# Kernel tuning notes

Hardware: AMD Instinct MI355X
Metric: run time of the kernel (lower is better)

Reference implementation:

```python
import jax, jax.numpy as jnp
import numpy as np

B, L, D, H = 8, 2048, 128, 128
MASK_VALUE = -1e30


def setup_inputs() -> dict:
    key = jax.random.key(0)
    ks = jax.random.split(key, 5)
    return {
        "query": jax.random.normal(ks[0], (B, L, D), dtype=jnp.float32),
        "key": jax.random.normal(ks[1], (B, L, D), dtype=jnp.float32),
        "value": jax.random.normal(ks[2], (B, L, D), dtype=jnp.float32),
        "mask": jnp.ones((B, L), dtype=jnp.float32),
        "Wq": jax.random.normal(ks[3], (D, H), dtype=jnp.float32) * (1.0 / np.sqrt(D)),
        "Wk": jax.random.normal(ks[4], (D, H), dtype=jnp.float32) * (1.0 / np.sqrt(D)),
    }


def reference(query, key, value, mask, Wq, Wk):
    # q: [B,Lq,H], k: [B,Lk,H]
    q = jnp.einsum("bqd,dh->bqh", query, Wq)
    k = jnp.einsum("bkd,dh->bkh", key, Wk)
    # unscaled scores [B,Lq,Lk]
    A = jnp.einsum("bqh,bkh->bqk", q, k)
    m = mask[:, None, :]  # [B,1,Lk]
    A = m * A + (1.0 - m) * MASK_VALUE
    # inference path: no dropout (learning_phase False)
    A = jax.nn.softmax(A, axis=-1)
    return jnp.einsum("bqk,bkd->bqd", A, value)
```

## Files before the change

kernel.cpp:

```cpp
#include <hip/hip_runtime.h>

#define NB 8
#define NL 2048
#define ND 128
#define NH 128
#define MASKVAL (-1e30f)
#define SHIFTC 40.0f

typedef __attribute__((ext_vector_type(8))) short short8;
typedef __attribute__((ext_vector_type(4))) float f32x4;

__device__ __forceinline__ unsigned short bf16_rn(float f) {
  unsigned u = __float_as_uint(f);
  u += 0x7fffu + ((u >> 16) & 1u);
  return (unsigned short)(u >> 16);
}
__device__ __forceinline__ float bf16_tof(unsigned short h) {
  return __uint_as_float(((unsigned)h) << 16);
}
__device__ __forceinline__ void gload16(const void* g, void* l) {
  __builtin_amdgcn_global_load_lds(
      (const __attribute__((address_space(1))) unsigned*)g,
      (__attribute__((address_space(3))) unsigned*)l, 16, 0, 0);
}


__global__ __launch_bounds__(256) void wprep_kernel(
    const float* __restrict__ Wq, const float* __restrict__ Wk,
    short* __restrict__ wthq, short* __restrict__ wtlq,
    short* __restrict__ wthk, short* __restrict__ wtlk)
{
  int m = blockIdx.x >> 4;
  int bb = blockIdx.x & 15;
  const float* W = m ? Wk : Wq;
  short* wth = m ? wthk : wthq;
  short* wtl = m ? wtlk : wtlq;
  int idx = bb * 256 + threadIdx.x;
  int d = idx >> 5, hc = idx & 31;
  float4 wv = *(const float4*)(W + d * NH + hc * 4);
  float vv[4] = {wv.x, wv.y, wv.z, wv.w};
#pragma unroll
  for (int j = 0; j < 4; ++j) {
    int h = hc * 4 + j;
    unsigned short hb = bf16_rn(vv[j]);
    unsigned short lb = bf16_rn(vv[j] - bf16_tof(hb));
    wth[h * ND + d] = (short)hb;
    wtl[h * ND + d] = (short)lb;
  }
}

__global__ __launch_bounds__(256) void vtprep_kernel(
    const float* __restrict__ value, short* __restrict__ kvs)
{
  __shared__ short Tl[64][66];
  __shared__ short VB[2][2048];
  int b = blockIdx.x >> 6;
  int k0 = ((blockIdx.x >> 1) & 31) * 64;
  int d0 = (blockIdx.x & 1) * 64;
  int t = threadIdx.x;
  int dm = t & 7, kp = t >> 3;
  float v0[8], v1[8];
  {
    const float* vp0 = value + (size_t)(b * NL + k0 + kp * 2) * ND + d0 + dm * 8;
    const float* vp1 = vp0 + ND;
    float4 a0 = *(const float4*)vp0;       float4 c0 = *(const float4*)(vp0 + 4);
    float4 a1 = *(const float4*)vp1;       float4 c1 = *(const float4*)(vp1 + 4);
    v0[0]=a0.x; v0[1]=a0.y; v0[2]=a0.z; v0[3]=a0.w; v0[4]=c0.x; v0[5]=c0.y; v0[6]=c0.z; v0[7]=c0.w;
    v1[0]=a1.x; v1[1]=a1.y; v1[2]=a1.z; v1[3]=a1.w; v1[4]=c1.x; v1[5]=c1.y; v1[6]=c1.z; v1[7]=c1.w;
  }
#pragma unroll
  for (int j = 0; j < 8; ++j) {
    unsigned pk = (unsigned)bf16_rn(v0[j]) | ((unsigned)bf16_rn(v1[j]) << 16);
    *(unsigned*)&Tl[dm * 8 + j][kp * 2] = pk;
  }
  __syncthreads();
  int dr = t >> 2, kc4 = t & 3;
  int d = d0 + dr;
  const unsigned* base = (const unsigned*)&Tl[dr][0];
  unsigned w[8];
#pragma unroll
  for (int i = 0; i < 8; ++i) w[i] = base[kc4 * 8 + i];
  int jt = kc4 >> 1;
  int kcg = (kc4 & 1) * 2;
  int g0 = ((d * 4 + kcg) ^ (d & 7)) - d0 * 4;
  int g1 = ((d * 4 + kcg + 1) ^ (d & 7)) - d0 * 4;
  *(uint4*)&VB[jt][g0 * 8] = make_uint4(w[0], w[1], w[2], w[3]);
  *(uint4*)&VB[jt][g1 * 8] = make_uint4(w[4], w[5], w[6], w[7]);
  __syncthreads();
  int kt = k0 >> 5;
#pragma unroll
  for (int c = 0; c < 2; ++c) {
    int idx = c * 256 + t;
    int j = idx >> 8, off = (idx & 255) * 8;
    *(uint4*)(kvs + (size_t)(b * 64 + kt + j) * 12288 + 8192 + d0 * 32 + off) =
        *(const uint4*)&VB[j][off];
  }
}

__global__ __launch_bounds__(256) void proj_kernel(
    const float* __restrict__ query, const float* __restrict__ key,
    const short* __restrict__ wthq, const short* __restrict__ wtlq,
    const short* __restrict__ wthk, const short* __restrict__ wtlk,
    unsigned* __restrict__ qhl, short* __restrict__ kvs)
{
  __shared__ short KB2[16384];
  const float* X = blockIdx.y ? key : query;
  const short* wth = blockIdx.y ? wthk : wthq;
  const short* wtl = blockIdx.y ? wtlk : wtlq;

  int tid = threadIdx.x;
  int wave = tid >> 6, lane = tid & 63;
  int lr = lane & 15, dg = lane >> 4;
  int arow = blockIdx.x * 64 + wave * 16 + lr;

  short8 ah[4], al[4];
  const float* xr = X + (size_t)arow * ND;
#pragma unroll
  for (int ks = 0; ks < 4; ++ks) {
    float4 a0 = *(const float4*)(xr + ks * 32 + dg * 8);
    float4 a1 = *(const float4*)(xr + ks * 32 + dg * 8 + 4);
    float vv[8] = {a0.x, a0.y, a0.z, a0.w, a1.x, a1.y, a1.z, a1.w};
    short8 h, l;
#pragma unroll
    for (int j = 0; j < 8; ++j) {
      unsigned short hb = bf16_rn(vv[j]);
      h[j] = (short)hb;
      l[j] = (short)bf16_rn(vv[j] - bf16_tof(hb));
    }
    ah[ks] = h; al[ks] = l;
  }

#pragma unroll
  for (int cf = 0; cf < 8; ++cf) {
    f32x4 acc = {0.f, 0.f, 0.f, 0.f};
    int col = cf * 16 + lr;
    const short* whp = wth + (size_t)col * ND;
    const short* wlp = wtl + (size_t)col * ND;
#pragma unroll
    for (int ks = 0; ks < 4; ++ks) {
      short8 wh = *(const short8*)(whp + ks * 32 + dg * 8);
      short8 wl = *(const short8*)(wlp + ks * 32 + dg * 8);
      acc = __builtin_amdgcn_mfma_f32_16x16x32_bf16(ah[ks], wh, acc, 0, 0, 0);
      acc = __builtin_amdgcn_mfma_f32_16x16x32_bf16(al[ks], wh, acc, 0, 0, 0);
      acc = __builtin_amdgcn_mfma_f32_16x16x32_bf16(ah[ks], wl, acc, 0, 0, 0);
    }
#pragma unroll
    for (int r = 0; r < 4; ++r) {
      int orow = blockIdx.x * 64 + wave * 16 + dg * 4 + r;
      float v = acc[r];
      unsigned short hb = bf16_rn(v);
      unsigned short lb = bf16_rn(v - bf16_tof(hb));
      if (blockIdx.y == 0) {
        qhl[(size_t)orow * NH + col] = ((unsigned)lb << 16) | (unsigned)hb;
      } else {
        int jj = (orow >> 5) & 1;
        int krow = orow & 31;
        int gr = krow * 128 + (((col >> 3) ^ (krow & 7)) * 8) + (col & 7);
        KB2[jj * 8192 + gr] = (short)hb;
        KB2[jj * 8192 + 4096 + gr] = (short)lb;
      }
    }
  }
  if (blockIdx.y == 1) {
    __syncthreads();
    int r0 = blockIdx.x * 64;
    int bb2 = r0 >> 11;
    int kt0 = (r0 & (NL - 1)) >> 5;
#pragma unroll
    for (int c = 0; c < 8; ++c) {
      int idx = c * 256 + tid;
      int j = idx >> 10, off = (idx & 1023) * 8;
      *(uint4*)(kvs + (size_t)(bb2 * 64 + kt0 + j) * 12288 + off) =
          *(const uint4*)&KB2[j * 8192 + off];
    }
  }
}

__global__ __launch_bounds__(256, 2) void attn_kernel(
    const unsigned* __restrict__ qhl, const short* __restrict__ kvs,
    const float* __restrict__ mask,
    unsigned short* __restrict__ pacc, float* __restrict__ pl)
{
  __shared__ short KV[2][12288];
  __shared__ float Msk[1024];
  __shared__ short Plds[4][16][32];

  int tid = threadIdx.x;
  int w = tid >> 6, lane = tid & 63;
  int lr = lane & 15, dg = lane >> 4;
  int b = blockIdx.x & 7;
  int qt = (blockIdx.x >> 3) & 31;
  int half = blockIdx.x >> 8;
  int q0 = qt * 64;

  short8 qh[4], ql[4];
  {
    const unsigned* qp = qhl + (size_t)(b * NL + q0 + w * 16 + lr) * NH;
#pragma unroll
    for (int ks = 0; ks < 4; ++ks) {
      uint4 u0 = *(const uint4*)(qp + ks * 32 + dg * 8);
      uint4 u1 = *(const uint4*)(qp + ks * 32 + dg * 8 + 4);
      unsigned uv[8] = {u0.x, u0.y, u0.z, u0.w, u1.x, u1.y, u1.z, u1.w};
      short8 h, l;
#pragma unroll
      for (int j = 0; j < 8; ++j) {
        h[j] = (short)(uv[j] & 0xffffu);
        l[j] = (short)(uv[j] >> 16);
      }
      qh[ks] = h; ql[ks] = l;
    }
  }

  gload16(mask + b * NL + half * 1024 + w * 256 + lane * 4, Msk + w * 256);

  f32x4 accv[8];
#pragma unroll
  for (int f = 0; f < 8; ++f) accv[f] = (f32x4){0.f, 0.f, 0.f, 0.f};
  float lrow[4] = {0.f, 0.f, 0.f, 0.f};

  const short* gbase = kvs + (size_t)(b * 64 + half * 32) * 12288 + w * 3072 + lane * 8;

#pragma unroll
  for (int i = 0; i < 6; ++i)
    gload16(gbase + i * 512, &KV[0][w * 3072 + i * 512]);

  for (int t = 0; t < 32; ++t) {
    __builtin_amdgcn_s_barrier();
    if (t + 1 < 32) {
      const short* gt = gbase + (size_t)(t + 1) * 12288;
      short* lt = &KV[(t + 1) & 1][w * 3072];
#pragma unroll
      for (int i = 0; i < 6; ++i)
        gload16(gt + i * 512, lt + i * 512);
      asm volatile("s_waitcnt vmcnt(6)" ::: "memory");
    } else {
      asm volatile("s_waitcnt vmcnt(0)" ::: "memory");
    }
    __builtin_amdgcn_s_barrier();
    __builtin_amdgcn_sched_barrier(0);

    const short* Kb = &KV[t & 1][0];
    f32x4 sc0 = {0.f, 0.f, 0.f, 0.f}, sc1 = {0.f, 0.f, 0.f, 0.f};
#pragma unroll
    for (int ks = 0; ks < 4; ++ks) {
      int chp = (((ks * 4 + dg) ^ (lr & 7)) * 8);
      short8 b0h = *(const short8*)(Kb + lr * 128 + chp);
      short8 b0l = *(const short8*)(Kb + 4096 + lr * 128 + chp);
      short8 b1h = *(const short8*)(Kb + (16 + lr) * 128 + chp);
      short8 b1l = *(const short8*)(Kb + 4096 + (16 + lr) * 128 + chp);
      sc0 = __builtin_amdgcn_mfma_f32_16x16x32_bf16(qh[ks], b0h, sc0, 0, 0, 0);
      sc1 = __builtin_amdgcn_mfma_f32_16x16x32_bf16(qh[ks], b1h, sc1, 0, 0, 0);
      sc0 = __builtin_amdgcn_mfma_f32_16x16x32_bf16(ql[ks], b0h, sc0, 0, 0, 0);
      sc1 = __builtin_amdgcn_mfma_f32_16x16x32_bf16(ql[ks], b1h, sc1, 0, 0, 0);
      sc0 = __builtin_amdgcn_mfma_f32_16x16x32_bf16(qh[ks], b0l, sc0, 0, 0, 0);
      sc1 = __builtin_amdgcn_mfma_f32_16x16x32_bf16(qh[ks], b1l, sc1, 0, 0, 0);
    }
    float mk0 = Msk[t * 32 + lr];
    float mk1 = Msk[t * 32 + 16 + lr];
#pragma unroll
    for (int r = 0; r < 4; ++r) {
      float s0 = mk0 * sc0[r] + (1.f - mk0) * MASKVAL - SHIFTC;
      float s1 = mk1 * sc1[r] + (1.f - mk1) * MASKVAL - SHIFTC;
      float p0 = __expf(s0);
      float p1 = __expf(s1);
      lrow[r] += p0 + p1;
      Plds[w][dg * 4 + r][lr] = (short)bf16_rn(p0);
      Plds[w][dg * 4 + r][16 + lr] = (short)bf16_rn(p1);
    }
    short8 pa = *(const short8*)&Plds[w][lr][dg * 8];
#pragma unroll
    for (int f = 0; f < 8; ++f) {
      int row = f * 16 + lr;
      int cp = (((row * 4 + dg) ^ (row & 7)) * 8);
      short8 bv = *(const short8*)(Kb + 8192 + cp);
      accv[f] = __builtin_amdgcn_mfma_f32_16x16x32_bf16(pa, bv, accv[f], 0, 0, 0);
    }
  }

#pragma unroll
  for (int r = 0; r < 4; ++r) {
    float lt = lrow[r];
    lt += __shfl_xor(lt, 1);
    lt += __shfl_xor(lt, 2);
    lt += __shfl_xor(lt, 4);
    lt += __shfl_xor(lt, 8);
    size_t grow = (size_t)b * NL + q0 + w * 16 + dg * 4 + r;
    if (lr == 0) pl[(size_t)half * (NB * NL) + grow] = lt;
    unsigned short* pb = pacc + ((size_t)half * (NB * NL) + grow) * ND;
#pragma unroll
    for (int f = 0; f < 8; ++f)
      pb[f * 16 + lr] = bf16_rn(accv[f][r]);
  }
}

__global__ __launch_bounds__(256) void merge_kernel(
    const unsigned short* __restrict__ pacc, const float* __restrict__ pl,
    float* __restrict__ out)
{
  int g = blockIdx.x * 256 + threadIdx.x;
  int row = g >> 4, ch = g & 15;
  float rinv = 1.f / (pl[row] + pl[NB * NL + row]);
  const unsigned short* a0 = pacc + (size_t)row * ND + ch * 8;
  const unsigned short* a1 = a0 + (size_t)(NB * NL) * ND;
  float* op = out + (size_t)row * ND + ch * 8;
#pragma unroll
  for (int j = 0; j < 8; ++j)
    op[j] = (bf16_tof(a0[j]) + bf16_tof(a1[j])) * rinv;
}

extern "C" void kernel_launch(void* const* d_in, const int* in_sizes, int n_in,
                              void* d_out, int out_size, void* d_ws, size_t ws_size,
                              hipStream_t stream) {
  (void)in_sizes; (void)n_in; (void)out_size; (void)ws_size;
  const float* query = (const float*)d_in[0];
  const float* key   = (const float*)d_in[1];
  const float* value = (const float*)d_in[2];
  const float* mask  = (const float*)d_in[3];
  const float* Wq    = (const float*)d_in[4];
  const float* Wk    = (const float*)d_in[5];
  float* out = (float*)d_out;

  char* ws = (char*)d_ws;
  short* wthq = (short*)(ws);
  short* wtlq = (short*)(ws + (32 << 10));
  short* wthk = (short*)(ws + (64 << 10));
  short* wtlk = (short*)(ws + (96 << 10));
  size_t off = 128 << 10;
  unsigned* qhl = (unsigned*)(ws + off);
  off += (size_t)8 << 20;
  short* kvs = (short*)(ws + off);
  off += (size_t)NB * 64 * 12288 * 2;
  unsigned short* pacc = (unsigned short*)(ws + off);
  off += (size_t)2 * NB * NL * ND * 2;
  float* pl = (float*)(ws + off);

  wprep_kernel<<<dim3(32), dim3(256), 0, stream>>>(Wq, Wk, wthq, wtlq, wthk, wtlk);
  vtprep_kernel<<<dim3(512), dim3(256), 0, stream>>>(value, kvs);
  proj_kernel<<<dim3(NB * NL / 64, 2), dim3(256), 0, stream>>>(
      query, key, wthq, wtlq, wthk, wtlk, qhl, kvs);
  attn_kernel<<<dim3(512), dim3(256), 0, stream>>>(qhl, kvs, mask, pacc, pl);
  merge_kernel<<<dim3(NB * NL * ND / (256 * 8)), dim3(256), 0, stream>>>(pacc, pl, out);
}
```

Measured before the change: 152.6 us.

## Split attention keys into more segments and keep P in registers via transposed MFMA

The attention kernel now takes a runtime segment count and picks 4 key segments when the workspace is large enough, otherwise 2. This doubles the grid so more blocks run per CU, and launch bounds are raised to 3 blocks per CU. The score MFMAs swap operand order so each lane's accumulator already matches the P operand layout for the PV MFMA, which removes the LDS round trip through Plds and the per-row shuffle reductions. The weight prep kernel and the value transpose kernel are reworked to use LDS-staged, coalesced stores. The cost is more bf16 partial accumulators to write and merge, plus possible register pressure at the higher occupancy target.

```diff
diff --git a/kernel.cpp b/kernel.cpp
--- a/kernel.cpp
+++ b/kernel.cpp
@@ -30,22 +30,32 @@
     short* __restrict__ wthq, short* __restrict__ wtlq,
     short* __restrict__ wthk, short* __restrict__ wtlk)
 {
-  int m = blockIdx.x >> 4;
-  int bb = blockIdx.x & 15;
+  __shared__ short Th[128][34];
+  __shared__ short Tll[128][34];
+  int m = blockIdx.x >> 2, dt = blockIdx.x & 3;
   const float* W = m ? Wk : Wq;
-  short* wth = m ? wthk : wthq;
-  short* wtl = m ? wtlk : wtlq;
-  int idx = bb * 256 + threadIdx.x;
-  int d = idx >> 5, hc = idx & 31;
-  float4 wv = *(const float4*)(W + d * NH + hc * 4);
-  float vv[4] = {wv.x, wv.y, wv.z, wv.w};
-#pragma unroll
-  for (int j = 0; j < 4; ++j) {
-    int h = hc * 4 + j;
-    unsigned short hb = bf16_rn(vv[j]);
-    unsigned short lb = bf16_rn(vv[j] - bf16_tof(hb));
-    wth[h * ND + d] = (short)hb;
-    wtl[h * ND + d] = (short)lb;
+  short* th = m ? wthk : wthq;
+  short* tl = m ? wtlk : wtlq;
+  int tid = threadIdx.x;
+#pragma unroll
+  for (int c = 0; c < 16; ++c) {
+    int idx = c * 256 + tid;
+    int dl = idx >> 7, h = idx & 127;
+    float v = W[(dt * 32 + dl) * NH + h];
+    unsigned short hb = bf16_rn(v);
+    Th[h][dl] = (short)hb;
+    Tll[h][dl] = (short)bf16_rn(v - bf16_tof(hb));
+  }
+  __syncthreads();
+#pragma unroll
+  for (int c = 0; c < 16; ++c) {
+    int idx = c * 256 + tid;
+    int plane = idx >> 11, rest = idx & 2047;
+    int h = rest >> 4, du = rest & 15;
+    unsigned v = plane ? *(const unsigned*)&Tll[h][du * 2]
+                       : *(const unsigned*)&Th[h][du * 2];
+    short* dst = plane ? tl : th;
+    *(unsigned*)&dst[h * ND + dt * 32 + du * 2] = v;
   }
 }
 
@@ -75,17 +85,18 @@
   }
   __syncthreads();
   int dr = t >> 2, kc4 = t & 3;
-  int d = d0 + dr;
   const unsigned* base = (const unsigned*)&Tl[dr][0];
   unsigned w[8];
 #pragma unroll
   for (int i = 0; i < 8; ++i) w[i] = base[kc4 * 8 + i];
-  int jt = kc4 >> 1;
-  int kcg = (kc4 & 1) * 2;
-  int g0 = ((d * 4 + kcg) ^ (d & 7)) - d0 * 4;
-  int g1 = ((d * 4 + kcg + 1) ^ (d & 7)) - d0 * 4;
-  *(uint4*)&VB[jt][g0 * 8] = make_uint4(w[0], w[1], w[2], w[3]);
-  *(uint4*)&VB[jt][g1 * 8] = make_uint4(w[4], w[5], w[6], w[7]);
+  int jt = kc4 >> 1, hh = kc4 & 1;
+#pragma unroll
+  for (int i = 0; i < 8; ++i) {
+    int g = i >> 1;
+    int lg = (dr * 4 + g) ^ (dr & 7);
+    int jslot = ((2 * i) & 3) + 4 * hh;
+    *(unsigned*)&VB[jt][lg * 8 + jslot] = w[i];
+  }
   __syncthreads();
   int kt = k0 >> 5;
 #pragma unroll
@@ -176,21 +187,21 @@
   }
 }
 
-__global__ __launch_bounds__(256, 2) void attn_kernel(
+__global__ __launch_bounds__(256, 3) void attn_kernel(
     const unsigned* __restrict__ qhl, const short* __restrict__ kvs,
     const float* __restrict__ mask,
-    unsigned short* __restrict__ pacc, float* __restrict__ pl)
+    unsigned short* __restrict__ pacc, float* __restrict__ pl,
+    int nseg, int tiles)
 {
   __shared__ short KV[2][12288];
   __shared__ float Msk[1024];
-  __shared__ short Plds[4][16][32];
 
   int tid = threadIdx.x;
   int w = tid >> 6, lane = tid & 63;
   int lr = lane & 15, dg = lane >> 4;
   int b = blockIdx.x & 7;
   int qt = (blockIdx.x >> 3) & 31;
-  int half = blockIdx.x >> 8;
+  int seg = blockIdx.x >> 8;
   int q0 = qt * 64;
 
   short8 qh[4], ql[4];
@@ -211,22 +222,25 @@
     }
   }
 
-  gload16(mask + b * NL + half * 1024 + w * 256 + lane * 4, Msk + w * 256);
+  int mwords = (NL / nseg) / 4;
+  if (lane * 4 < mwords)
+    gload16(mask + b * NL + seg * (NL / nseg) + w * mwords + lane * 4,
+            Msk + w * mwords);
 
   f32x4 accv[8];
 #pragma unroll
   for (int f = 0; f < 8; ++f) accv[f] = (f32x4){0.f, 0.f, 0.f, 0.f};
-  float lrow[4] = {0.f, 0.f, 0.f, 0.f};
-
-  const short* gbase = kvs + (size_t)(b * 64 + half * 32) * 12288 + w * 3072 + lane * 8;
+  float lsum = 0.f;
+
+  const short* gbase = kvs + (size_t)(b * 64 + seg * tiles) * 12288 + w * 3072 + lane * 8;
 
 #pragma unroll
   for (int i = 0; i < 6; ++i)
     gload16(gbase + i * 512, &KV[0][w * 3072 + i * 512]);
 
-  for (int t = 0; t < 32; ++t) {
+  for (int t = 0; t < tiles; ++t) {
     __builtin_amdgcn_s_barrier();
-    if (t + 1 < 32) {
+    if (t + 1 < tiles) {
       const short* gt = gbase + (size_t)(t + 1) * 12288;
       short* lt = &KV[(t + 1) & 1][w * 3072];
 #pragma unroll
@@ -248,26 +262,29 @@
       short8 b0l = *(const short8*)(Kb + 4096 + lr * 128 + chp);
       short8 b1h = *(const short8*)(Kb + (16 + lr) * 128 + chp);
       short8 b1l = *(const short8*)(Kb + 4096 + (16 + lr) * 128 + chp);
-      sc0 = __builtin_amdgcn_mfma_f32_16x16x32_bf16(qh[ks], b0h, sc0, 0, 0, 0);
-      sc1 = __builtin_amdgcn_mfma_f32_16x16x32_bf16(qh[ks], b1h, sc1, 0, 0, 0);
-      sc0 = __builtin_amdgcn_mfma_f32_16x16x32_bf16(ql[ks], b0h, sc0, 0, 0, 0);
-      sc1 = __builtin_amdgcn_mfma_f32_16x16x32_bf16(ql[ks], b1h, sc1, 0, 0, 0);
-      sc0 = __builtin_amdgcn_mfma_f32_16x16x32_bf16(qh[ks], b0l, sc0, 0, 0, 0);
-      sc1 = __builtin_amdgcn_mfma_f32_16x16x32_bf16(qh[ks], b1l, sc1, 0, 0, 0);
-    }
-    float mk0 = Msk[t * 32 + lr];
-    float mk1 = Msk[t * 32 + 16 + lr];
+      sc0 = __builtin_amdgcn_mfma_f32_16x16x32_bf16(b0h, qh[ks], sc0, 0, 0, 0);
+      sc1 = __builtin_amdgcn_mfma_f32_16x16x32_bf16(b1h, qh[ks], sc1, 0, 0, 0);
+      sc0 = __builtin_amdgcn_mfma_f32_16x16x32_bf16(b0l, qh[ks], sc0, 0, 0, 0);
+      sc1 = __builtin_amdgcn_mfma_f32_16x16x32_bf16(b1l, qh[ks], sc1, 0, 0, 0);
+      sc0 = __builtin_amdgcn_mfma_f32_16x16x32_bf16(b0h, ql[ks], sc0, 0, 0, 0);
+      sc1 = __builtin_amdgcn_mfma_f32_16x16x32_bf16(b1h, ql[ks], sc1, 0, 0, 0);
+    }
+    float4 mk0 = *(const float4*)&Msk[t * 32 + dg * 4];
+    float4 mk1 = *(const float4*)&Msk[t * 32 + 16 + dg * 4];
+    float m0a[4] = {mk0.x, mk0.y, mk0.z, mk0.w};
+    float m1a[4] = {mk1.x, mk1.y, mk1.z, mk1.w};
+    short8 pa;
+    float ps = 0.f;
 #pragma unroll
     for (int r = 0; r < 4; ++r) {
-      float s0 = mk0 * sc0[r] + (1.f - mk0) * MASKVAL - SHIFTC;
-      float s1 = mk1 * sc1[r] + (1.f - mk1) * MASKVAL - SHIFTC;
-      float p0 = __expf(s0);
-      float p1 = __expf(s1);
-      lrow[r] += p0 + p1;
-      Plds[w][dg * 4 + r][lr] = (short)bf16_rn(p0);
-      Plds[w][dg * 4 + r][16 + lr] = (short)bf16_rn(p1);
-    }
-    short8 pa = *(const short8*)&Plds[w][lr][dg * 8];
+      float s0 = m0a[r] * sc0[r] + (1.f - m0a[r]) * MASKVAL - SHIFTC;
+      float s1 = m1a[r] * sc1[r] + (1.f - m1a[r]) * MASKVAL - SHIFTC;
+      float p0 = __expf(s0), p1 = __expf(s1);
+      ps += p0 + p1;
+      pa[r] = (short)bf16_rn(p0);
+      pa[4 + r] = (short)bf16_rn(p1);
+    }
+    lsum += ps;
 #pragma unroll
     for (int f = 0; f < 8; ++f) {
       int row = f * 16 + lr;
@@ -277,16 +294,15 @@
     }
   }
 
+  lsum += __shfl_xor(lsum, 16);
+  lsum += __shfl_xor(lsum, 32);
+  size_t segbase = (size_t)seg * (NB * NL);
+  if (lane < 16)
+    pl[segbase + b * NL + q0 + w * 16 + lr] = lsum;
 #pragma unroll
   for (int r = 0; r < 4; ++r) {
-    float lt = lrow[r];
-    lt += __shfl_xor(lt, 1);
-    lt += __shfl_xor(lt, 2);
-    lt += __shfl_xor(lt, 4);
-    lt += __shfl_xor(lt, 8);
-    size_t grow = (size_t)b * NL + q0 + w * 16 + dg * 4 + r;
-    if (lr == 0) pl[(size_t)half * (NB * NL) + grow] = lt;
-    unsigned short* pb = pacc + ((size_t)half * (NB * NL) + grow) * ND;
+    size_t grow = segbase + b * NL + q0 + w * 16 + dg * 4 + r;
+    unsigned short* pb = pacc + grow * ND;
 #pragma unroll
     for (int f = 0; f < 8; ++f)
       pb[f * 16 + lr] = bf16_rn(accv[f][r]);
@@ -295,23 +311,28 @@
 
 __global__ __launch_bounds__(256) void merge_kernel(
     const unsigned short* __restrict__ pacc, const float* __restrict__ pl,
-    float* __restrict__ out)
+    float* __restrict__ out, int nseg)
 {
   int g = blockIdx.x * 256 + threadIdx.x;
   int row = g >> 4, ch = g & 15;
-  float rinv = 1.f / (pl[row] + pl[NB * NL + row]);
-  const unsigned short* a0 = pacc + (size_t)row * ND + ch * 8;
-  const unsigned short* a1 = a0 + (size_t)(NB * NL) * ND;
+  float ls = 0.f;
+  for (int s = 0; s < nseg; ++s) ls += pl[(size_t)s * (NB * NL) + row];
+  float rinv = 1.f / ls;
+  float acc[8] = {0.f, 0.f, 0.f, 0.f, 0.f, 0.f, 0.f, 0.f};
+  for (int s = 0; s < nseg; ++s) {
+    const unsigned short* a = pacc + ((size_t)s * (NB * NL) + row) * ND + ch * 8;
+#pragma unroll
+    for (int j = 0; j < 8; ++j) acc[j] += bf16_tof(a[j]);
+  }
   float* op = out + (size_t)row * ND + ch * 8;
 #pragma unroll
-  for (int j = 0; j < 8; ++j)
-    op[j] = (bf16_tof(a0[j]) + bf16_tof(a1[j])) * rinv;
+  for (int j = 0; j < 8; ++j) op[j] = acc[j] * rinv;
 }
 
 extern "C" void kernel_launch(void* const* d_in, const int* in_sizes, int n_in,
                               void* d_out, int out_size, void* d_ws, size_t ws_size,
                               hipStream_t stream) {
-  (void)in_sizes; (void)n_in; (void)out_size; (void)ws_size;
+  (void)in_sizes; (void)n_in; (void)out_size;
   const float* query = (const float*)d_in[0];
   const float* key   = (const float*)d_in[1];
   const float* value = (const float*)d_in[2];
@@ -319,6 +340,9 @@
   const float* Wq    = (const float*)d_in[4];
   const float* Wk    = (const float*)d_in[5];
   float* out = (float*)d_out;
+
+  int nseg = (ws_size >= ((size_t)40 << 20)) ? 4 : 2;
+  int tiles = NL / nseg / 32;
 
   char* ws = (char*)d_ws;
   short* wthq = (short*)(ws);
@@ -331,13 +355,15 @@
   short* kvs = (short*)(ws + off);
   off += (size_t)NB * 64 * 12288 * 2;
   unsigned short* pacc = (unsigned short*)(ws + off);
-  off += (size_t)2 * NB * NL * ND * 2;
+  off += (size_t)nseg * NB * NL * ND * 2;
   float* pl = (float*)(ws + off);
 
-  wprep_kernel<<<dim3(32), dim3(256), 0, stream>>>(Wq, Wk, wthq, wtlq, wthk, wtlk);
+  wprep_kernel<<<dim3(8), dim3(256), 0, stream>>>(Wq, Wk, wthq, wtlq, wthk, wtlk);
   vtprep_kernel<<<dim3(512), dim3(256), 0, stream>>>(value, kvs);
   proj_kernel<<<dim3(NB * NL / 64, 2), dim3(256), 0, stream>>>(
       query, key, wthq, wtlq, wthk, wtlk, qhl, kvs);
-  attn_kernel<<<dim3(512), dim3(256), 0, stream>>>(qhl, kvs, mask, pacc, pl);
-  merge_kernel<<<dim3(NB * NL * ND / (256 * 8)), dim3(256), 0, stream>>>(pacc, pl, out);
-}
+  attn_kernel<<<dim3(256 * nseg), dim3(256), 0, stream>>>(
+      qhl, kvs, mask, pacc, pl, nseg, tiles);
+  merge_kernel<<<dim3(NB * NL * ND / (256 * 8)), dim3(256), 0, stream>>>(
+      pacc, pl, out, nseg);
+}
```

New measurement: 153.8 us. No clear change (+0.8%).
